# Optimization experiments

Hardware: AMD Instinct MI355X
Metric: run time of the kernel (lower is better)

Reference implementation:

```python
import jax, jax.numpy as jnp
import numpy as np
from jax import lax

V, H, M, OD, NL, S, B, KS = 32000, 1024, 16, 16, 4, 512, 16, 3
N = H // M          # 64
DN = OD * N         # 1024 (layernorm dim)
EPS = 1e-5


def _layernorm(x, g, b):
    mu = jnp.mean(x, axis=-1, keepdims=True)
    var = jnp.var(x, axis=-1, keepdims=True)
    return (x - mu) * lax.rsqrt(var + EPS) * g + b


def _conv(x, w, b):
    y = lax.conv_general_dilated(x, w, (1, 1), 'SAME',
                                 dimension_numbers=('NCHW', 'OIHW', 'NCHW'))
    return y + b[None, :, None, None]


def setup_inputs() -> dict:
    key = jax.random.key(0)
    ks = jax.random.split(key, 16)
    inp = {
        'x': jax.random.randint(ks[0], (B, S), 0, V),
        'emb_table': jax.random.normal(ks[1], (V, H), jnp.float32) * 0.02,
        'ln0_g': jnp.ones((H,), jnp.float32),
        'ln0_b': jnp.zeros((H,), jnp.float32),
        'qw': jax.random.normal(ks[2], (NL, OD, M, KS, KS), jnp.float32) * 0.05,
        'qb': jnp.zeros((NL, OD), jnp.float32),
        'kw': jax.random.normal(ks[3], (NL, OD, M, KS, KS), jnp.float32) * 0.05,
        'kb': jnp.zeros((NL, OD), jnp.float32),
        'vw': jax.random.normal(ks[4], (NL, OD, M, KS, KS), jnp.float32) * 0.05,
        'vb': jnp.zeros((NL, OD), jnp.float32),
        'lng': jnp.ones((NL, DN), jnp.float32),
        'lnb': jnp.zeros((NL, DN), jnp.float32),
        'cw': jax.random.normal(ks[5], (NL, M, OD, 3, 3), jnp.float32) * 0.05,
        'cb': jnp.zeros((NL, M), jnp.float32),
    }
    return inp


def reference(x, emb_table, ln0_g, ln0_b, qw, qb, kw, kb, vw, vb, lng, lnb, cw, cb):
    gelu = lambda t: jax.nn.gelu(t, approximate=False)  # torch nn.GELU default (erf)
    # embedding with padding_idx=0 (row forced to zero)
    table = emb_table.at[0].set(0.0)
    h = _layernorm(table[x], ln0_g, ln0_b)              # [B,S,H]
    h = h.reshape(B, S, M, N).transpose(0, 2, 1, 3)      # [B,M,S,N]
    outs = ()
    for i in range(NL):
        outs = outs + (h,)
        q = gelu(_conv(h, qw[i], qb[i]))                 # [B,OD,S,N]
        k = gelu(_conv(h, kw[i], kb[i]))
        v = gelu(_conv(h, vw[i], vb[i]))
        q2 = q.transpose(0, 2, 1, 3).reshape(B, S, DN)   # [B,S,OD*N]
        k2 = k.transpose(0, 1, 3, 2).reshape(B, DN, S)   # [B,OD*N,S]
        v2 = v.transpose(0, 2, 1, 3).reshape(B, S, DN)
        score = jax.nn.softmax(jnp.matmul(q2, k2), axis=0)  # softmax over batch (dim=0)
        o = jnp.matmul(score, v2)                        # [B,S,DN]
        o = _layernorm(o, lng[i], lnb[i])
        o = o.reshape(B, S, OD, N).transpose(0, 2, 1, 3)  # [B,OD,S,N]
        h = gelu(_conv(o, cw[i], cb[i])) + h             # residual, [B,M,S,N]
    return (h,) + outs
```

## Files before the change

kernel.cpp:

```cpp
#include <hip/hip_runtime.h>
#include <hip/hip_bf16.h>

typedef unsigned short u16;
typedef unsigned int   u32;
typedef short bf16x8 __attribute__((ext_vector_type(8)));
typedef float f32x4  __attribute__((ext_vector_type(4)));

#define SS 512
#define XSWZ(g)     ((((g) & 7) << 6) | ((g) >> 3))
#define XSWZ1024(g) ((((g) & 7) << 7) | ((g) >> 3))
#define WPREP_STRIDE 22016

__device__ __forceinline__ float gelu_f(float v){
    float x  = v * 0.70710678118654752f;
    float ax = fabsf(x);
    float t  = __builtin_amdgcn_rcpf(fmaf(0.3275911f, ax, 1.0f));
    float poly = t*(0.254829592f + t*(-0.284496736f + t*(1.421413741f
               + t*(-1.453152027f + t*1.061405429f))));
    float e  = __expf(-x*x);
    float er = copysignf(1.0f - poly*e, x);
    return 0.5f*v*(1.0f + er);
}
__device__ __forceinline__ u16 bf16_rne(float v){
    u32 u = __float_as_uint(v);
    u32 r = u + 0x7FFF + ((u >> 16) & 1);
    return (u16)(r >> 16);
}
#define DYT(t) ((t)>=9 ? 0 : (t)/3)
#define DXT(t) ((t)>=9 ? 0 : (t)%3)

__global__ __launch_bounds__(256) void k_prep(
    const float* __restrict__ qw, const float* __restrict__ kw,
    const float* __restrict__ vw, const float* __restrict__ cw,
    const float* __restrict__ lng, const float* __restrict__ lnb,
    u16* __restrict__ wprep)
{
    int L = blockIdx.x;
    int tid = threadIdx.x;
    u16* base = wprep + L*WPREP_STRIDE;
    const float* src[4] = {qw + L*2304, kw + L*2304, vw + L*2304, cw + L*2304};
    const int offh[4] = {0, 5120, 10240, 12800};
    const int offl[4] = {2560, 7680, -1, 15360};
    for (int idx = tid; idx < 2304; idx += 256){
        int o = idx / 144, rem = idx - o*144;
        int i = rem / 9, tap = rem - i*9;
        int dst = o*160 + tap*16 + i;
        #pragma unroll
        for (int a = 0; a < 4; ++a){
            float wv = src[a][idx];
            u16 hv = bf16_rne(wv);
            base[offh[a] + dst] = hv;
            if (offl[a] >= 0)
                base[offl[a] + dst] = bf16_rne(wv - __uint_as_float((u32)hv<<16));
        }
    }
    {
        int o = tid >> 4, kk = tid & 15;
        int d = o*160 + 144 + kk;
        base[d]=0; base[2560+d]=0; base[5120+d]=0; base[7680+d]=0;
        base[10240+d]=0; base[12800+d]=0; base[15360+d]=0;
    }
    float* gr = (float*)(base + 17920);
    float* br = (float*)(base + 19968);
    for (int idx = tid; idx < 1024; idx += 256){
        int od = (idx & 15)*64 + (idx >> 4);
        gr[idx] = lng[L*1024 + od];
        br[idx] = lnb[L*1024 + od];
    }
}

__global__ __launch_bounds__(256) void k_embed_ln(
    const int* __restrict__ x, const float* __restrict__ emb,
    const float* __restrict__ g, const float* __restrict__ bta,
    float* __restrict__ h, u16* __restrict__ hh, u16* __restrict__ hl)
{
    int bs = blockIdx.x;
    int b = bs >> 9, s = bs & 511;
    int t = x[bs];
    int tid = threadIdx.x;
    float v[4];
    #pragma unroll
    for (int j = 0; j < 4; ++j){
        int idx = tid + j*256;
        v[j] = (t == 0) ? 0.0f : emb[(size_t)t*1024 + idx];
    }
    float sum = v[0]+v[1]+v[2]+v[3];
    float sq  = v[0]*v[0]+v[1]*v[1]+v[2]*v[2]+v[3]*v[3];
    __shared__ float red[2][4];
    int lane = tid & 63, wid = tid >> 6;
    #pragma unroll
    for (int off = 32; off; off >>= 1){
        sum += __shfl_down(sum, off, 64);
        sq  += __shfl_down(sq,  off, 64);
    }
    if (lane == 0){ red[0][wid] = sum; red[1][wid] = sq; }
    __syncthreads();
    sum = red[0][0]+red[0][1]+red[0][2]+red[0][3];
    sq  = red[1][0]+red[1][1]+red[1][2]+red[1][3];
    float mean = sum * (1.0f/1024.0f);
    float var  = sq  * (1.0f/1024.0f) - mean*mean;
    float rs = rsqrtf(var + 1e-5f);
    #pragma unroll
    for (int j = 0; j < 4; ++j){
        int idx = tid + j*256;
        float y = (v[j]-mean)*rs*g[idx] + bta[idx];
        int m = idx >> 6, n = idx & 63;
        h[((size_t)(b*16 + m)*SS + s)*64 + n] = y;
        u16 hv = bf16_rne(y);
        u16 lv = bf16_rne(y - __uint_as_float((u32)hv<<16));
        size_t da = ((size_t)b*SS + s)*1024 + n*16 + m;
        hh[da] = hv; hl[da] = lv;
    }
}

__global__ __launch_bounds__(256,2) void k_conv_qkv(
    const u16* __restrict__ inh, const u16* __restrict__ inl,
    const u16* __restrict__ wp,
    const float* __restrict__ qb, const float* __restrict__ kb,
    const float* __restrict__ vb,
    u16* __restrict__ qoh, u16* __restrict__ qol,
    u16* __restrict__ koh, u16* __restrict__ kol,
    u16* __restrict__ vT)
{
    int bid = XSWZ1024(blockIdx.x);
    int b  = bid >> 6;
    int y0 = (bid & 63) * 8;
    int tid = threadIdx.x;
    int w4 = tid >> 6, lane = tid & 63;
    int l15 = lane & 15, l4 = lane >> 4;

    __shared__ u16 shi[10*68*24];
    __shared__ u16 slo[10*68*24];

    if (tid < 40){
        int y = tid >> 2, rr = tid & 3;
        int tc = (rr >> 1) ? 65 : 0;
        int h8 = (rr & 1) * 8;
        int ad = (y*68 + tc)*24 + h8;
        *(uint4*)&shi[ad] = make_uint4(0,0,0,0);
        *(uint4*)&slo[ad] = make_uint4(0,0,0,0);
    }
    #pragma unroll
    for (int it = 0; it < 5; ++it){
        int idx = tid + it*256;
        int y = idx >> 7;
        int rem = idx & 127;
        int xx = rem >> 1, h8 = (rem & 1)*8;
        int gy = y0 - 1 + y;
        uint4 vh = make_uint4(0,0,0,0), vl = make_uint4(0,0,0,0);
        if (gy >= 0 && gy < SS){
            size_t ga = ((size_t)b*SS + gy)*1024 + xx*16 + h8;
            vh = *(const uint4*)(inh + ga);
            vl = *(const uint4*)(inl + ga);
        }
        int la = (y*68 + (xx+1))*24 + h8;
        *(uint4*)&shi[la] = vh;
        *(uint4*)&slo[la] = vl;
    }
    __syncthreads();

    bf16x8 aq_h[5], aq_l[5], ak_h[5], ak_l[5], av_h[5];
    #pragma unroll
    for (int p = 0; p < 5; ++p){
        int aad = l15*160 + p*32 + l4*8;
        aq_h[p] = *(const bf16x8*)&wp[aad];
        aq_l[p] = *(const bf16x8*)&wp[2560 + aad];
        ak_h[p] = *(const bf16x8*)&wp[5120 + aad];
        ak_l[p] = *(const bf16x8*)&wp[7680 + aad];
        av_h[p] = *(const bf16x8*)&wp[10240 + aad];
    }

    f32x4 accq[8], acck[8], accv[8];
    #pragma unroll
    for (int i = 0; i < 8; ++i){
        accq[i] = (f32x4){0.f,0.f,0.f,0.f};
        acck[i] = (f32x4){0.f,0.f,0.f,0.f};
        accv[i] = (f32x4){0.f,0.f,0.f,0.f};
    }
    int hsel = l4 >> 1;
    int i0 = (l4 & 1)*8;
    int xo = w4*16 + l15;

    #pragma unroll
    for (int p = 0; p < 5; ++p){
        int dy = hsel ? DYT(2*p+1) : DYT(2*p);
        int dx = hsel ? DXT(2*p+1) : DXT(2*p);
        int badd0 = (dy*68 + xo + dx)*24 + i0;
        #pragma unroll
        for (int yy = 0; yy < 8; ++yy){
            int bad = badd0 + yy*(68*24);
            bf16x8 bh = *(const bf16x8*)&shi[bad];
            bf16x8 bl = *(const bf16x8*)&slo[bad];
            accq[yy] = __builtin_amdgcn_mfma_f32_16x16x32_bf16(aq_h[p], bh, accq[yy],0,0,0);
            accq[yy] = __builtin_amdgcn_mfma_f32_16x16x32_bf16(aq_l[p], bh, accq[yy],0,0,0);
            accq[yy] = __builtin_amdgcn_mfma_f32_16x16x32_bf16(aq_h[p], bl, accq[yy],0,0,0);
            acck[yy] = __builtin_amdgcn_mfma_f32_16x16x32_bf16(ak_h[p], bh, acck[yy],0,0,0);
            acck[yy] = __builtin_amdgcn_mfma_f32_16x16x32_bf16(ak_l[p], bh, acck[yy],0,0,0);
            acck[yy] = __builtin_amdgcn_mfma_f32_16x16x32_bf16(ak_h[p], bl, acck[yy],0,0,0);
            accv[yy] = __builtin_amdgcn_mfma_f32_16x16x32_bf16(av_h[p], bh, accv[yy],0,0,0);
        }
    }

    float qbv[4], kbv[4], vbv[4];
    #pragma unroll
    for (int i = 0; i < 4; ++i){
        qbv[i] = qb[l4*4 + i];
        kbv[i] = kb[l4*4 + i];
        vbv[i] = vb[l4*4 + i];
    }
    union { u16 u[4][8]; uint4 q[4]; } vpk;
    #pragma unroll
    for (int yy = 0; yy < 8; ++yy){
        int y = y0 + yy;
        u16 qh4[4], ql4[4], kh4[4], kl4[4];
        #pragma unroll
        for (int i = 0; i < 4; ++i){
            float vq = gelu_f(accq[yy][i] + qbv[i]);
            u16 hv = bf16_rne(vq);
            qh4[i] = hv; ql4[i] = bf16_rne(vq - __uint_as_float((u32)hv<<16));
            float vk = gelu_f(acck[yy][i] + kbv[i]);
            u16 kv = bf16_rne(vk);
            kh4[i] = kv; kl4[i] = bf16_rne(vk - __uint_as_float((u32)kv<<16));
            vpk.u[i][yy] = bf16_rne(gelu_f(accv[yy][i] + vbv[i]));
        }
        size_t oa = ((size_t)b*SS + y)*1024 + xo*16 + l4*4;
        *(uint2*)&qoh[oa] = make_uint2((u32)qh4[0]|((u32)qh4[1]<<16),(u32)qh4[2]|((u32)qh4[3]<<16));
        *(uint2*)&qol[oa] = make_uint2((u32)ql4[0]|((u32)ql4[1]<<16),(u32)ql4[2]|((u32)ql4[3]<<16));
        *(uint2*)&koh[oa] = make_uint2((u32)kh4[0]|((u32)kh4[1]<<16),(u32)kh4[2]|((u32)kh4[3]<<16));
        *(uint2*)&kol[oa] = make_uint2((u32)kl4[0]|((u32)kl4[1]<<16),(u32)kl4[2]|((u32)kl4[3]<<16));
    }
    #pragma unroll
    for (int i = 0; i < 4; ++i)
        *(uint4*)(vT + ((size_t)b*1024 + xo*16 + l4*4 + i)*SS + y0) = vpk.q[i];
}

__global__ __launch_bounds__(512,1) void k_conv_ln_res2(
    const float* __restrict__ o_pre, const float* __restrict__ stats,
    const u16* __restrict__ wp, const float* __restrict__ bias,
    const float* __restrict__ resid, float* __restrict__ outf,
    u16* __restrict__ outh, u16* __restrict__ outl)
{
    int bid = XSWZ(blockIdx.x);
    int b  = bid >> 5;
    int y0 = (bid & 31) * 16;
    int tid = threadIdx.x;
    int w8 = tid >> 6, lane = tid & 63;
    int l15 = lane & 15, l4 = lane >> 4;
    int xt = w8 & 3, yh8 = (w8 >> 2) * 8;

    __shared__ __align__(16) u16 whi[2560], wlo[2560];
    __shared__ u16 shi[18*68*24], slo[18*68*24];
    __shared__ __align__(16) float grem[1024], brem[1024];
    __shared__ float smu[18], srs[18];

    if (tid < 320){
        ((uint4*)whi)[tid] = ((const uint4*)(wp + 12800))[tid];
        ((uint4*)wlo)[tid] = ((const uint4*)(wp + 15360))[tid];
    }
    if (tid < 256){
        ((float4*)grem)[tid] = ((const float4*)(wp + 17920))[tid];
        ((float4*)brem)[tid] = ((const float4*)(wp + 19968))[tid];
    }
    if (tid < 18){
        int gy = y0 - 1 + tid;
        float mu = 0.f, rs = 0.f;
        if (gy >= 0 && gy < SS){
            float s = stats[2*((size_t)b*SS + gy)];
            float q = stats[2*((size_t)b*SS + gy) + 1];
            mu = s * (1.0f/1024.0f);
            float var = q * (1.0f/1024.0f) - mu*mu;
            rs = rsqrtf(var + 1e-5f);
        }
        smu[tid] = mu; srs[tid] = rs;
    }
    if (tid >= 64 && tid < 136){
        int t2 = tid - 64;
        int y = t2 >> 2, rr = t2 & 3;
        int tc = (rr >> 1) ? 65 : 0;
        int h8 = (rr & 1) * 8;
        int ad = (y*68 + tc)*24 + h8;
        *(uint4*)&shi[ad] = make_uint4(0,0,0,0);
        *(uint4*)&slo[ad] = make_uint4(0,0,0,0);
    }
    __syncthreads();

    for (int idx = tid; idx < 4608; idx += 512){
        int y = idx >> 8;
        int rem = idx & 255;
        int xx = rem >> 2, cq = (rem & 3)*4;
        int gy = y0 - 1 + y;
        int la = (y*68 + xx + 1)*24 + cq;
        if (gy >= 0 && gy < SS){
            float4 vv = *(const float4*)(o_pre + ((size_t)b*SS + gy)*1024 + xx*16 + cq);
            float mu = smu[y], rs = srs[y];
            int dbase = xx*16 + cq;
            float va[4] = {vv.x, vv.y, vv.z, vv.w};
            u16 hh4[4], ll4[4];
            #pragma unroll
            for (int j = 0; j < 4; ++j){
                float yv = (va[j] - mu)*rs*grem[dbase + j] + brem[dbase + j];
                hh4[j] = bf16_rne(yv);
                ll4[j] = bf16_rne(yv - __uint_as_float((u32)hh4[j]<<16));
            }
            *(uint2*)&shi[la] = make_uint2((u32)hh4[0]|((u32)hh4[1]<<16),(u32)hh4[2]|((u32)hh4[3]<<16));
            *(uint2*)&slo[la] = make_uint2((u32)ll4[0]|((u32)ll4[1]<<16),(u32)ll4[2]|((u32)ll4[3]<<16));
        } else {
            *(uint2*)&shi[la] = make_uint2(0,0);
            *(uint2*)&slo[la] = make_uint2(0,0);
        }
    }
    __syncthreads();

    bf16x8 ah[5], al[5];
    #pragma unroll
    for (int p = 0; p < 5; ++p){
        int aad = l15*160 + p*32 + l4*8;
        ah[p] = *(const bf16x8*)&whi[aad];
        al[p] = *(const bf16x8*)&wlo[aad];
    }

    f32x4 acc[8];
    #pragma unroll
    for (int i = 0; i < 8; ++i) acc[i] = (f32x4){0.f,0.f,0.f,0.f};
    int hsel = l4 >> 1;
    int i0 = (l4 & 1)*8;
    int xo = xt*16 + l15;

    #pragma unroll
    for (int p = 0; p < 5; ++p){
        int dy = hsel ? DYT(2*p+1) : DYT(2*p);
        int dx = hsel ? DXT(2*p+1) : DXT(2*p);
        int badd0 = ((dy + yh8)*68 + xo + dx)*24 + i0;
        #pragma unroll
        for (int yy = 0; yy < 8; ++yy){
            int bad = badd0 + yy*(68*24);
            bf16x8 bh = *(const bf16x8*)&shi[bad];
            bf16x8 bl = *(const bf16x8*)&slo[bad];
            acc[yy] = __builtin_amdgcn_mfma_f32_16x16x32_bf16(ah[p], bh, acc[yy],0,0,0);
            acc[yy] = __builtin_amdgcn_mfma_f32_16x16x32_bf16(al[p], bh, acc[yy],0,0,0);
            acc[yy] = __builtin_amdgcn_mfma_f32_16x16x32_bf16(ah[p], bl, acc[yy],0,0,0);
        }
    }

    float bv[4];
    #pragma unroll
    for (int i = 0; i < 4; ++i) bv[i] = bias[l4*4 + i];
    #pragma unroll
    for (int yy = 0; yy < 8; ++yy){
        int y = y0 + yh8 + yy;
        float r[4];
        #pragma unroll
        for (int i = 0; i < 4; ++i) r[i] = gelu_f(acc[yy][i] + bv[i]);
        #pragma unroll
        for (int i = 0; i < 4; ++i){
            int o = l4*4 + i;
            size_t fa = ((size_t)(b*16 + o)*SS + y)*64 + xo;
            float hv = resid[fa] + r[i];
            outf[fa] = hv;
            r[i] = hv;
        }
        u16 hh_[4], ll_[4];
        #pragma unroll
        for (int i = 0; i < 4; ++i){
            hh_[i] = bf16_rne(r[i]);
            ll_[i] = bf16_rne(r[i] - __uint_as_float((u32)hh_[i]<<16));
        }
        size_t oa = ((size_t)b*SS + y)*1024 + xo*16 + l4*4;
        *(uint2*)&outh[oa] = make_uint2((u32)hh_[0]|((u32)hh_[1]<<16),(u32)hh_[2]|((u32)hh_[3]<<16));
        *(uint2*)&outl[oa] = make_uint2((u32)ll_[0]|((u32)ll_[1]<<16),(u32)ll_[2]|((u32)ll_[3]<<16));
    }
}

__global__ __launch_bounds__(256) void k_qk_mfma(
    const u16* __restrict__ qh, const u16* __restrict__ ql,
    const u16* __restrict__ kh, const u16* __restrict__ kl,
    float* __restrict__ score)
{
    int bid = XSWZ(blockIdx.x);
    int b = bid >> 5;
    int s1_0 = ((bid >> 3) & 3) * 128;
    int s2_0 = (bid & 7) * 64;
    __shared__ u16 Ah[128*64], Al[128*64], Bh[64*64], Bl[64*64];
    int tid = threadIdx.x;
    int w = tid >> 6, lane = tid & 63;
    int l15 = lane & 15, l4 = lane >> 4;
    f32x4 acc[2][4];
    #pragma unroll
    for (int r=0;r<2;++r)
        #pragma unroll
        for(int c=0;c<4;++c) acc[r][c] = (f32x4){0.f,0.f,0.f,0.f};

    for (int oc = 0; oc < 16; ++oc){
        size_t qbase = ((size_t)b*SS + s1_0)*1024 + oc*64;
        size_t kbase = ((size_t)b*SS + s2_0)*1024 + oc*64;
        #pragma unroll
        for (int i = 0; i < 4; ++i){
            int idx = tid + i*256;
            int r = idx >> 3, f = idx & 7;
            int dst = r*64 + ((f ^ (r & 7))*8);
            *(uint4*)&Ah[dst] = *(const uint4*)(qh + qbase + (size_t)r*1024 + f*8);
            *(uint4*)&Al[dst] = *(const uint4*)(ql + qbase + (size_t)r*1024 + f*8);
        }
        #pragma unroll
        for (int i = 0; i < 2; ++i){
            int idx = tid + i*256;
            int r = idx >> 3, f = idx & 7;
            int dst = r*64 + ((f ^ (r & 7))*8);
            *(uint4*)&Bh[dst] = *(const uint4*)(kh + kbase + (size_t)r*1024 + f*8);
            *(uint4*)&Bl[dst] = *(const uint4*)(kl + kbase + (size_t)r*1024 + f*8);
        }
        __syncthreads();
        #pragma unroll
        for (int ks = 0; ks < 2; ++ks){
            bf16x8 a_h[2], a_l[2];
            #pragma unroll
            for (int r=0;r<2;++r){
                int row = w*32 + r*16 + l15;
                int ad = row*64 + (((ks*4 + l4) ^ (row & 7))*8);
                a_h[r] = *(const bf16x8*)&Ah[ad];
                a_l[r] = *(const bf16x8*)&Al[ad];
            }
            #pragma unroll
            for (int c=0;c<4;++c){
                int row = c*16 + l15;
                int bd = row*64 + (((ks*4 + l4) ^ (row & 7))*8);
                bf16x8 b_h = *(const bf16x8*)&Bh[bd];
                bf16x8 b_l = *(const bf16x8*)&Bl[bd];
                #pragma unroll
                for (int r=0;r<2;++r){
                    acc[r][c] = __builtin_amdgcn_mfma_f32_16x16x32_bf16(a_h[r], b_h, acc[r][c],0,0,0);
                    acc[r][c] = __builtin_amdgcn_mfma_f32_16x16x32_bf16(a_l[r], b_h, acc[r][c],0,0,0);
                    acc[r][c] = __builtin_amdgcn_mfma_f32_16x16x32_bf16(a_h[r], b_l, acc[r][c],0,0,0);
                }
            }
        }
        __syncthreads();
    }
    #pragma unroll
    for (int r=0;r<2;++r)
        #pragma unroll
        for (int c=0;c<4;++c)
            #pragma unroll
            for (int i=0;i<4;++i){
                int s1 = s1_0 + w*32 + r*16 + l4*4 + i;
                int s2 = s2_0 + c*16 + l15;
                score[((size_t)b*SS + s1)*SS + s2] = acc[r][c][i];
            }
}

__global__ __launch_bounds__(256) void k_softmax_b(
    const float* __restrict__ score, u16* __restrict__ scb,
    float* __restrict__ stats)
{
    int sid = blockIdx.x*256 + threadIdx.x;
    if (sid < 16384) stats[sid] = 0.0f;
    float vals[16];
    float m = -1e30f;
    #pragma unroll
    for (int b = 0; b < 16; ++b){
        vals[b] = score[(size_t)b*SS*SS + sid];
        m = fmaxf(m, vals[b]);
    }
    float sum = 0.f;
    #pragma unroll
    for (int b = 0; b < 16; ++b){ vals[b] = __expf(vals[b]-m); sum += vals[b]; }
    float inv = 1.0f/sum;
    #pragma unroll
    for (int b = 0; b < 16; ++b) scb[(size_t)b*SS*SS + sid] = bf16_rne(vals[b]*inv);
}

__global__ __launch_bounds__(256) void k_sv_mfma(
    const u16* __restrict__ scb, const u16* __restrict__ vT,
    float* __restrict__ o, float* __restrict__ stats)
{
    int bid = XSWZ(blockIdx.x);
    int b = bid >> 5;
    int s1_0 = ((bid >> 3) & 3) * 128;
    int d0 = (bid & 7) * 128;
    __shared__ u16 As[128*64], Bs[128*64];
    int tid = threadIdx.x;
    int w = tid >> 6, lane = tid & 63;
    int l15 = lane & 15, l4 = lane >> 4;
    f32x4 acc[2][8];
    #pragma unroll
    for (int r=0;r<2;++r)
        #pragma unroll
        for(int c=0;c<8;++c) acc[r][c] = (f32x4){0.f,0.f,0.f,0.f};

    for (int st = 0; st < 8; ++st){
        int s2b = st*64;
        #pragma unroll
        for (int i = 0; i < 4; ++i){
            int idx = tid + i*256;
            int r = idx >> 3, f = idx & 7;
            int dst = r*64 + ((f ^ (r & 7))*8);
            *(uint4*)&As[dst] = *(const uint4*)(scb + ((size_t)b*SS + s1_0 + r)*SS + s2b + f*8);
            *(uint4*)&Bs[dst] = *(const uint4*)(vT + ((size_t)b*1024 + d0 + r)*SS + s2b + f*8);
        }
        __syncthreads();
        #pragma unroll
        for (int ks = 0; ks < 2; ++ks){
            bf16x8 a0[2];
            #pragma unroll
            for (int r=0;r<2;++r){
                int row = w*32 + r*16 + l15;
                a0[r] = *(const bf16x8*)&As[row*64 + (((ks*4 + l4) ^ (row & 7))*8)];
            }
            #pragma unroll
            for (int c=0;c<8;++c){
                int row = c*16 + l15;
                bf16x8 b0 = *(const bf16x8*)&Bs[row*64 + (((ks*4 + l4) ^ (row & 7))*8)];
                #pragma unroll
                for (int r=0;r<2;++r)
                    acc[r][c] = __builtin_amdgcn_mfma_f32_16x16x32_bf16(a0[r], b0, acc[r][c],0,0,0);
            }
        }
        __syncthreads();
    }
    #pragma unroll
    for (int r=0;r<2;++r)
        #pragma unroll
        for (int c=0;c<8;++c)
            #pragma unroll
            for (int i=0;i<4;++i){
                int s1 = s1_0 + w*32 + r*16 + l4*4 + i;
                o[((size_t)b*SS + s1)*1024 + d0 + c*16 + l15] = acc[r][c][i];
            }

    #pragma unroll
    for (int r=0;r<2;++r){
        #pragma unroll
        for (int i=0;i<4;++i){
            float s = 0.f, q = 0.f;
            #pragma unroll
            for (int c=0;c<8;++c){ float v = acc[r][c][i]; s += v; q += v*v; }
            #pragma unroll
            for (int m = 1; m <= 8; m <<= 1){
                s += __shfl_xor(s, m, 64);
                q += __shfl_xor(q, m, 64);
            }
            if (l15 == 0){
                int s1 = s1_0 + w*32 + r*16 + l4*4 + i;
                atomicAdd(&stats[2*((size_t)b*SS + s1)],     s);
                atomicAdd(&stats[2*((size_t)b*SS + s1) + 1], q);
            }
        }
    }
}

extern "C" void kernel_launch(void* const* d_in, const int* in_sizes, int n_in,
                              void* d_out, int out_size, void* d_ws, size_t ws_size,
                              hipStream_t stream)
{
    const int*   x    = (const int*)  d_in[0];
    const float* emb  = (const float*)d_in[1];
    const float* g0   = (const float*)d_in[2];
    const float* b0   = (const float*)d_in[3];
    const float* qw   = (const float*)d_in[4];
    const float* qb   = (const float*)d_in[5];
    const float* kw   = (const float*)d_in[6];
    const float* kb   = (const float*)d_in[7];
    const float* vw   = (const float*)d_in[8];
    const float* vb_  = (const float*)d_in[9];
    const float* lng  = (const float*)d_in[10];
    const float* lnb  = (const float*)d_in[11];
    const float* cw   = (const float*)d_in[12];
    const float* cb   = (const float*)d_in[13];
    float* out = (float*)d_out;

    const size_t TS = (size_t)16*16*512*64;
    u16* wsu = (u16*)d_ws;
    u16* hh = wsu + 0*TS;
    u16* hl = wsu + 1*TS;
    u16* qh = wsu + 2*TS;
    u16* ql = wsu + 3*TS;
    u16* kh = wsu + 4*TS;
    u16* kl = wsu + 5*TS;
    u16* vT = wsu + 6*TS;
    float* sc    = (float*)(wsu + 7*TS);
    u16*   scb   = qh;
    float* o_pre = (float*)(wsu + 4*TS);
    float* stats = (float*)(wsu + 3*TS);
    u16* wprep = (u16*)((char*)d_ws + ((size_t)160 << 20));

    float* hbuf[5];
    hbuf[0] = out + 1*TS;
    hbuf[1] = out + 2*TS;
    hbuf[2] = out + 3*TS;
    hbuf[3] = out + 4*TS;
    hbuf[4] = out;

    k_prep<<<4, 256, 0, stream>>>(qw, kw, vw, cw, lng, lnb, wprep);
    k_embed_ln<<<8192, 256, 0, stream>>>(x, emb, g0, b0, hbuf[0], hh, hl);
    for (int i = 0; i < 4; ++i){
        const u16* wp = wprep + i*WPREP_STRIDE;
        k_conv_qkv<<<1024, 256, 0, stream>>>(
            hh, hl, wp, qb + i*16, kb + i*16, vb_ + i*16, qh, ql, kh, kl, vT);
        k_qk_mfma<<<512, 256, 0, stream>>>(qh, ql, kh, kl, sc);
        k_softmax_b<<<1024, 256, 0, stream>>>(sc, scb, stats);
        k_sv_mfma<<<512, 256, 0, stream>>>(scb, vT, o_pre, stats);
        k_conv_ln_res2<<<512, 512, 0, stream>>>(
            o_pre, stats, wp, cb + i*16, hbuf[i], hbuf[i+1], hh, hl);
    }
}
```

Baseline: 579.4 us.

## Split conv-LN-residual kernel into smaller 8-row blocks with direct weight loads

The output-conv kernel now uses 256-thread blocks covering 8 rows instead of 512-thread blocks covering 16 rows, doubling the grid to 1024 blocks and allowing two blocks per CU. Conv weights, gamma and beta are read straight from global memory instead of being staged in shared memory. Per-row LN statistics are computed inline, and the halo fill uses 8-wide vector loads and stores. This is meant to cut shared-memory footprint and the staging barrier and to raise occupancy, at the cost of more halo rows loaded redundantly (10 per 8 rows versus 18 per 16) and repeated global weight reads.

```diff
diff --git a/kernel.cpp b/kernel.cpp
--- a/kernel.cpp
+++ b/kernel.cpp
@@ -234,80 +234,70 @@
         *(uint4*)(vT + ((size_t)b*1024 + xo*16 + l4*4 + i)*SS + y0) = vpk.q[i];
 }
 
-__global__ __launch_bounds__(512,1) void k_conv_ln_res2(
+__global__ __launch_bounds__(256,2) void k_conv_ln_res2(
     const float* __restrict__ o_pre, const float* __restrict__ stats,
     const u16* __restrict__ wp, const float* __restrict__ bias,
     const float* __restrict__ resid, float* __restrict__ outf,
     u16* __restrict__ outh, u16* __restrict__ outl)
 {
-    int bid = XSWZ(blockIdx.x);
-    int b  = bid >> 5;
-    int y0 = (bid & 31) * 16;
+    int bid = XSWZ1024(blockIdx.x);
+    int b  = bid >> 6;
+    int y0 = (bid & 63) * 8;
     int tid = threadIdx.x;
-    int w8 = tid >> 6, lane = tid & 63;
+    int w4 = tid >> 6, lane = tid & 63;
     int l15 = lane & 15, l4 = lane >> 4;
-    int xt = w8 & 3, yh8 = (w8 >> 2) * 8;
-
-    __shared__ __align__(16) u16 whi[2560], wlo[2560];
-    __shared__ u16 shi[18*68*24], slo[18*68*24];
-    __shared__ __align__(16) float grem[1024], brem[1024];
-    __shared__ float smu[18], srs[18];
-
-    if (tid < 320){
-        ((uint4*)whi)[tid] = ((const uint4*)(wp + 12800))[tid];
-        ((uint4*)wlo)[tid] = ((const uint4*)(wp + 15360))[tid];
-    }
-    if (tid < 256){
-        ((float4*)grem)[tid] = ((const float4*)(wp + 17920))[tid];
-        ((float4*)brem)[tid] = ((const float4*)(wp + 19968))[tid];
-    }
-    if (tid < 18){
-        int gy = y0 - 1 + tid;
-        float mu = 0.f, rs = 0.f;
-        if (gy >= 0 && gy < SS){
-            float s = stats[2*((size_t)b*SS + gy)];
-            float q = stats[2*((size_t)b*SS + gy) + 1];
-            mu = s * (1.0f/1024.0f);
-            float var = q * (1.0f/1024.0f) - mu*mu;
-            rs = rsqrtf(var + 1e-5f);
-        }
-        smu[tid] = mu; srs[tid] = rs;
-    }
-    if (tid >= 64 && tid < 136){
-        int t2 = tid - 64;
-        int y = t2 >> 2, rr = t2 & 3;
+
+    __shared__ u16 shi[10*68*24];
+    __shared__ u16 slo[10*68*24];
+
+    if (tid < 40){
+        int y = tid >> 2, rr = tid & 3;
         int tc = (rr >> 1) ? 65 : 0;
         int h8 = (rr & 1) * 8;
         int ad = (y*68 + tc)*24 + h8;
         *(uint4*)&shi[ad] = make_uint4(0,0,0,0);
         *(uint4*)&slo[ad] = make_uint4(0,0,0,0);
     }
-    __syncthreads();
-
-    for (int idx = tid; idx < 4608; idx += 512){
-        int y = idx >> 8;
-        int rem = idx & 255;
-        int xx = rem >> 2, cq = (rem & 3)*4;
+    const float* gr = (const float*)(wp + 17920);
+    const float* br = (const float*)(wp + 19968);
+    #pragma unroll
+    for (int it = 0; it < 5; ++it){
+        int idx = tid + it*256;
+        int y = idx >> 7;
+        int rem = idx & 127;
+        int xx = rem >> 1, h8 = (rem & 1)*8;
         int gy = y0 - 1 + y;
-        int la = (y*68 + xx + 1)*24 + cq;
+        int la = (y*68 + (xx+1))*24 + h8;
+        uint4 ph = make_uint4(0,0,0,0), pl = make_uint4(0,0,0,0);
         if (gy >= 0 && gy < SS){
-            float4 vv = *(const float4*)(o_pre + ((size_t)b*SS + gy)*1024 + xx*16 + cq);
-            float mu = smu[y], rs = srs[y];
-            int dbase = xx*16 + cq;
-            float va[4] = {vv.x, vv.y, vv.z, vv.w};
-            u16 hh4[4], ll4[4];
-            #pragma unroll
-            for (int j = 0; j < 4; ++j){
-                float yv = (va[j] - mu)*rs*grem[dbase + j] + brem[dbase + j];
-                hh4[j] = bf16_rne(yv);
-                ll4[j] = bf16_rne(yv - __uint_as_float((u32)hh4[j]<<16));
-            }
-            *(uint2*)&shi[la] = make_uint2((u32)hh4[0]|((u32)hh4[1]<<16),(u32)hh4[2]|((u32)hh4[3]<<16));
-            *(uint2*)&slo[la] = make_uint2((u32)ll4[0]|((u32)ll4[1]<<16),(u32)ll4[2]|((u32)ll4[3]<<16));
-        } else {
-            *(uint2*)&shi[la] = make_uint2(0,0);
-            *(uint2*)&slo[la] = make_uint2(0,0);
-        }
+            float s  = stats[2*((size_t)b*SS + gy)];
+            float q  = stats[2*((size_t)b*SS + gy) + 1];
+            float mu = s * (1.0f/1024.0f);
+            float rs = rsqrtf(q * (1.0f/1024.0f) - mu*mu + 1e-5f);
+            int dbase = xx*16 + h8;
+            float4 v0 = *(const float4*)(o_pre + ((size_t)b*SS + gy)*1024 + dbase);
+            float4 v1 = *(const float4*)(o_pre + ((size_t)b*SS + gy)*1024 + dbase + 4);
+            float4 g0 = *(const float4*)&gr[dbase];
+            float4 g1 = *(const float4*)&gr[dbase + 4];
+            float4 b0 = *(const float4*)&br[dbase];
+            float4 b1 = *(const float4*)&br[dbase + 4];
+            float va[8] = {v0.x,v0.y,v0.z,v0.w,v1.x,v1.y,v1.z,v1.w};
+            float ga[8] = {g0.x,g0.y,g0.z,g0.w,g1.x,g1.y,g1.z,g1.w};
+            float ba[8] = {b0.x,b0.y,b0.z,b0.w,b1.x,b1.y,b1.z,b1.w};
+            u16 hh8[8], ll8[8];
+            #pragma unroll
+            for (int j = 0; j < 8; ++j){
+                float yv = (va[j] - mu)*rs*ga[j] + ba[j];
+                hh8[j] = bf16_rne(yv);
+                ll8[j] = bf16_rne(yv - __uint_as_float((u32)hh8[j]<<16));
+            }
+            ph = make_uint4((u32)hh8[0]|((u32)hh8[1]<<16), (u32)hh8[2]|((u32)hh8[3]<<16),
+                            (u32)hh8[4]|((u32)hh8[5]<<16), (u32)hh8[6]|((u32)hh8[7]<<16));
+            pl = make_uint4((u32)ll8[0]|((u32)ll8[1]<<16), (u32)ll8[2]|((u32)ll8[3]<<16),
+                            (u32)ll8[4]|((u32)ll8[5]<<16), (u32)ll8[6]|((u32)ll8[7]<<16));
+        }
+        *(uint4*)&shi[la] = ph;
+        *(uint4*)&slo[la] = pl;
     }
     __syncthreads();
 
@@ -315,8 +305,8 @@
     #pragma unroll
     for (int p = 0; p < 5; ++p){
         int aad = l15*160 + p*32 + l4*8;
-        ah[p] = *(const bf16x8*)&whi[aad];
-        al[p] = *(const bf16x8*)&wlo[aad];
+        ah[p] = *(const bf16x8*)&wp[12800 + aad];
+        al[p] = *(const bf16x8*)&wp[15360 + aad];
     }
 
     f32x4 acc[8];
@@ -324,13 +314,13 @@
     for (int i = 0; i < 8; ++i) acc[i] = (f32x4){0.f,0.f,0.f,0.f};
     int hsel = l4 >> 1;
     int i0 = (l4 & 1)*8;
-    int xo = xt*16 + l15;
+    int xo = w4*16 + l15;
 
     #pragma unroll
     for (int p = 0; p < 5; ++p){
         int dy = hsel ? DYT(2*p+1) : DYT(2*p);
         int dx = hsel ? DXT(2*p+1) : DXT(2*p);
-        int badd0 = ((dy + yh8)*68 + xo + dx)*24 + i0;
+        int badd0 = (dy*68 + xo + dx)*24 + i0;
         #pragma unroll
         for (int yy = 0; yy < 8; ++yy){
             int bad = badd0 + yy*(68*24);
@@ -347,7 +337,7 @@
     for (int i = 0; i < 4; ++i) bv[i] = bias[l4*4 + i];
     #pragma unroll
     for (int yy = 0; yy < 8; ++yy){
-        int y = y0 + yh8 + yy;
+        int y = y0 + yy;
         float r[4];
         #pragma unroll
         for (int i = 0; i < 4; ++i) r[i] = gelu_f(acc[yy][i] + bv[i]);
@@ -599,7 +589,7 @@
         k_qk_mfma<<<512, 256, 0, stream>>>(qh, ql, kh, kl, sc);
         k_softmax_b<<<1024, 256, 0, stream>>>(sc, scb, stats);
         k_sv_mfma<<<512, 256, 0, stream>>>(scb, vT, o_pre, stats);
-        k_conv_ln_res2<<<512, 512, 0, stream>>>(
+        k_conv_ln_res2<<<1024, 256, 0, stream>>>(
             o_pre, stats, wp, cb + i*16, hbuf[i], hbuf[i+1], hh, hl);
     }
 }
```

After: 572.0 us. No clear change (-1.3%).
